# Performance work log

Measured on AMD Instinct MI355X. Metric: run time of the kernel, lower is better.

## Reference

```python
import jax, jax.numpy as jnp
import numpy as np

N_NODES = 200000
N_EDGES = 640000
D_NODE = 128   # NO_NODE_FEATURES_TWO
D_EDGE = 32    # NO_EDGE_FEATURES_TWO
HIDDEN = 128   # HIDDEN_NODE_TWO


def setup_inputs() -> dict:
    key = jax.random.key(0)
    ks = jax.random.split(key, 8)
    x = jax.random.normal(ks[0], (N_NODES, D_NODE), dtype=jnp.float32)
    edge_index = jax.random.randint(ks[1], (2, N_EDGES), 0, N_NODES, dtype=jnp.int64)
    edge_attr = jax.random.normal(ks[2], (N_EDGES, D_EDGE), dtype=jnp.float32)
    u = jax.random.normal(ks[3], (64, D_NODE), dtype=jnp.float32)
    batch = jax.random.randint(ks[4], (N_NODES,), 0, 64, dtype=jnp.int64)
    # Xavier-uniform linear weights (stored as [in, out]); bias filled with 0.01 as in init_weights
    def xavier(k, fan_in, fan_out):
        limit = float(np.sqrt(6.0 / (fan_in + fan_out)))
        return jax.random.uniform(k, (fan_in, fan_out), jnp.float32, -limit, limit)
    W1 = xavier(ks[5], D_EDGE + D_NODE, HIDDEN)          # [160, 128]
    b1 = jnp.full((HIDDEN,), 0.01, dtype=jnp.float32)
    W2 = xavier(ks[6], HIDDEN + D_NODE, D_NODE)          # [256, 128]
    b2 = jnp.full((D_NODE,), 0.01, dtype=jnp.float32)
    return {"x": x, "edge_index": edge_index, "edge_attr": edge_attr,
            "u": u, "batch": batch, "W1": W1, "b1": b1, "W2": W2, "b2": b2}


def reference(x, edge_index, edge_attr, u, batch, W1, b1, W2, b2):
    row, col = edge_index[0], edge_index[1]
    # gather source-node features, concat with edge features: [E, 160]
    msg = jnp.concatenate([x[row], edge_attr], axis=1)
    msg = msg @ W1 + b1                                   # [E, hidden]
    # scatter_add by destination node
    agg = jax.ops.segment_sum(msg, col, num_segments=x.shape[0])  # [N, hidden]
    out = jnp.concatenate([x, agg], axis=1)               # [N, 256]
    return out @ W2 + b2                                  # [N, 128]
```

## Files before the change

kernel.cpp:

```cpp
#include <hip/hip_runtime.h>
#include <hip/hip_bf16.h>

#define N_NODES 200000
#define N_EDGES 640000
#define D_NODE 128
#define D_EDGE 32
#define HIDDEN 128
#define KTOT 288

using bf16x8  = __attribute__((ext_vector_type(8))) short;
using f32x4   = __attribute__((ext_vector_type(4))) float;
using short4v = __attribute__((ext_vector_type(4))) short;

__device__ __forceinline__ short f2b(float f) {
  return __builtin_bit_cast(short, __float2bfloat16(f));
}
__device__ __forceinline__ float b2f(short s) {
  unsigned u = ((unsigned)(unsigned short)s) << 16;
  return __builtin_bit_cast(float, u);
}

__global__ __launch_bounds__(256) void k_prep_x(const float* __restrict__ x,
                                                short* __restrict__ AF) {
  const int i = blockIdx.x * 256 + threadIdx.x;
  const int node = i >> 4;
  const int oct  = (i & 15) << 3;
  const float4 v0 = *(const float4*)&x[(size_t)node * D_NODE + oct];
  const float4 v1 = *(const float4*)&x[(size_t)node * D_NODE + oct + 4];
  bf16x8 o = { f2b(v0.x), f2b(v0.y), f2b(v0.z), f2b(v0.w),
               f2b(v1.x), f2b(v1.y), f2b(v1.z), f2b(v1.w) };
  *(bf16x8*)&AF[(size_t)node * KTOT + oct] = o;
}

__global__ __launch_bounds__(128) void k_prep_wc(const float* __restrict__ W1,
                                                 const float* __restrict__ b1,
                                                 const float* __restrict__ W2,
                                                 short* __restrict__ WcT,
                                                 float* __restrict__ bc) {
  const int b = blockIdx.x;
  const int c = threadIdx.x;
  if (b < 128) {
    WcT[c * KTOT + b] = f2b(W2[b * 128 + c]);
  } else if (b < KTOT) {
    const int i = b - 128;
    float acc = 0.f;
    #pragma unroll 8
    for (int q = 0; q < 128; ++q)
      acc += W1[i * 128 + q] * W2[(128 + q) * 128 + c];
    WcT[c * KTOT + b] = f2b(acc);
  } else {
    float acc = 0.f;
    #pragma unroll 8
    for (int q = 0; q < 128; ++q)
      acc += b1[q] * W2[(128 + q) * 128 + c];
    bc[c] = acc;
  }
}

__global__ __launch_bounds__(256) void k_hist(const int* __restrict__ ei,
                                              int* cnt, int* slot) {
  const int e = blockIdx.x * 256 + threadIdx.x;
  if (e < N_EDGES) slot[e] = atomicAdd(&cnt[ei[N_EDGES + e]], 1);
}

#define SCAN_NB 196

__global__ __launch_bounds__(256) void k_scan_a(const int* __restrict__ cnt,
                                                int* bsum) {
  __shared__ int sh[256];
  const int b = blockIdx.x, t = threadIdx.x;
  const int base = b * 1024 + t * 4;
  int s = 0;
  #pragma unroll
  for (int k = 0; k < 4; ++k) {
    const int idx = base + k;
    s += (idx < N_NODES) ? cnt[idx] : 0;
  }
  sh[t] = s; __syncthreads();
  for (int o = 128; o > 0; o >>= 1) {
    if (t < o) sh[t] += sh[t + o];
    __syncthreads();
  }
  if (t == 0) bsum[b] = sh[0];
}

__global__ __launch_bounds__(256) void k_scan_b(const int* __restrict__ bsum,
                                                int* bpre) {
  __shared__ int sh[256];
  const int t = threadIdx.x;
  const int v0 = (t < SCAN_NB) ? bsum[t] : 0;
  sh[t] = v0; __syncthreads();
  for (int o = 1; o < 256; o <<= 1) {
    const int tv = (t >= o) ? sh[t - o] : 0;
    __syncthreads();
    sh[t] += tv;
    __syncthreads();
  }
  bpre[t] = sh[t] - v0;
}

__global__ __launch_bounds__(256) void k_scan_c(const int* __restrict__ cnt,
                                                const int* __restrict__ bpre,
                                                int* offv) {
  __shared__ int sh[256];
  const int b = blockIdx.x, t = threadIdx.x;
  const int base = b * 1024 + t * 4;
  int v[4], p[4], s = 0;
  #pragma unroll
  for (int k = 0; k < 4; ++k) {
    const int idx = base + k;
    v[k] = (idx < N_NODES) ? cnt[idx] : 0;
    p[k] = s; s += v[k];
  }
  sh[t] = s; __syncthreads();
  const int tot = s;
  for (int o = 1; o < 256; o <<= 1) {
    const int tv = (t >= o) ? sh[t - o] : 0;
    __syncthreads();
    sh[t] += tv;
    __syncthreads();
  }
  const int gb = bpre[b] + (sh[t] - tot);
  #pragma unroll
  for (int k = 0; k < 4; ++k) {
    const int idx = base + k;
    if (idx < N_NODES) offv[idx] = gb + p[k];
  }
}

__global__ __launch_bounds__(256) void k_place2(const int* __restrict__ ei,
                                                const int* __restrict__ offv,
                                                const int* __restrict__ slot,
                                                int* perm, int* rows) {
  const int e = blockIdx.x * 256 + threadIdx.x;
  if (e < N_EDGES) {
    const int j = offv[ei[N_EDGES + e]] + slot[e];
    perm[j] = e;
    rows[j] = ei[e];
  }
}

__global__ __launch_bounds__(256) void k_sagg(
    const float* __restrict__ ea, const int* __restrict__ offv,
    const int* __restrict__ cnt, const int* __restrict__ rows,
    const int* __restrict__ perm, short* __restrict__ AF)
{
  const int gtid = blockIdx.x * 256 + threadIdx.x;
  if (gtid < N_NODES * 16) {
    const int node = gtid >> 4;
    const int oct  = (gtid & 15) << 3;
    const int s0 = offv[node];
    const int s1 = s0 + cnt[node];
    float a[8] = {};
    for (int j = s0; j < s1; ++j) {
      const int row = rows[j];
      const bf16x8 v = *(const bf16x8*)&AF[(size_t)row * KTOT + oct];
      #pragma unroll
      for (int k = 0; k < 8; ++k) a[k] += b2f(v[k]);
    }
    bf16x8 o;
    #pragma unroll
    for (int k = 0; k < 8; ++k) o[k] = f2b(a[k]);
    *(bf16x8*)&AF[(size_t)node * KTOT + 128 + oct] = o;
  } else {
    const int t2 = gtid - N_NODES * 16;
    const int node = t2 >> 3;
    const int q    = (t2 & 7) << 2;
    if (node >= N_NODES) return;
    const int s0 = offv[node];
    const int s1 = s0 + cnt[node];
    float a0 = 0.f, a1 = 0.f, a2 = 0.f, a3 = 0.f;
    for (int j = s0; j < s1; ++j) {
      const int e = perm[j];
      const float4 v = *(const float4*)&ea[(size_t)e * D_EDGE + q];
      a0 += v.x; a1 += v.y; a2 += v.z; a3 += v.w;
    }
    short4v o = { f2b(a0), f2b(a1), f2b(a2), f2b(a3) };
    *(short4v*)&AF[(size_t)node * KTOT + 256 + q] = o;
  }
}

#define LDP 104

__global__ __launch_bounds__(256, 4) void k_out2(
    const short* __restrict__ AF, const short* __restrict__ WcT,
    const float* __restrict__ bc, const float* __restrict__ b2,
    const int* __restrict__ cnt, float* __restrict__ out)
{
  __shared__ short smem[64 * LDP + 128 * LDP];
  short* lA = smem;
  short* lB = smem + 64 * LDP;
  const int tid = threadIdx.x;
  const int n0  = blockIdx.x * 64;

  const int lane = tid & 63;
  const int wid  = tid >> 6;
  const int wm = wid >> 1, wn = wid & 1;
  const int lrow = lane & 15;
  const int lk   = (lane >> 4) << 3;

  f32x4 acc[2][4] = {};

  #pragma unroll
  for (int p = 0; p < 3; ++p) {
    for (int i = tid; i < 1536; i += 256) {
      const int n = i / 12, ck = (i % 12) << 3;
      *(bf16x8*)&lB[n * LDP + ck] = *(const bf16x8*)&WcT[n * KTOT + p * 96 + ck];
    }
    for (int i = tid; i < 768; i += 256) {
      const int m = i / 12, ck = (i % 12) << 3;
      *(bf16x8*)&lA[m * LDP + ck] = *(const bf16x8*)&AF[(size_t)(n0 + m) * KTOT + p * 96 + ck];
    }
    __syncthreads();
    #pragma unroll
    for (int kt = 0; kt < 3; ++kt) {
      const int ks = kt * 32 + lk;
      bf16x8 af[2], bfr[4];
      #pragma unroll
      for (int i = 0; i < 2; ++i)
        af[i]  = *(const bf16x8*)&lA[(wm * 32 + i * 16 + lrow) * LDP + ks];
      #pragma unroll
      for (int j = 0; j < 4; ++j)
        bfr[j] = *(const bf16x8*)&lB[(wn * 64 + j * 16 + lrow) * LDP + ks];
      #pragma unroll
      for (int i = 0; i < 2; ++i)
        #pragma unroll
        for (int j = 0; j < 4; ++j)
          acc[i][j] = __builtin_amdgcn_mfma_f32_16x16x32_bf16(af[i], bfr[j], acc[i][j], 0, 0, 0);
    }
    __syncthreads();
  }

  float* lf = (float*)smem;
  const int rb = wm * 32 + ((lane >> 4) << 2);
  const int cb = wn * 64 + lrow;
  float bcv[4], b2v[4];
  #pragma unroll
  for (int j = 0; j < 4; ++j) {
    bcv[j] = bc[cb + j * 16];
    b2v[j] = b2[cb + j * 16];
  }
  #pragma unroll
  for (int i = 0; i < 2; ++i) {
    #pragma unroll
    for (int r = 0; r < 4; ++r) {
      const int row = rb + i * 16 + r;
      const float cf = (float)cnt[n0 + row];
      #pragma unroll
      for (int j = 0; j < 4; ++j)
        lf[row * 128 + cb + j * 16] = acc[i][j][r] + cf * bcv[j] + b2v[j];
    }
  }
  __syncthreads();
  #pragma unroll
  for (int u = 0; u < 8; ++u) {
    const int idx = tid + u * 256;
    const int row = idx >> 5, f4 = (idx & 31) << 2;
    *(float4*)&out[(size_t)(n0 + row) * HIDDEN + f4] = *(const float4*)&lf[row * 128 + f4];
  }
}

extern "C" void kernel_launch(void* const* d_in, const int* in_sizes, int n_in,
                              void* d_out, int out_size, void* d_ws, size_t ws_size,
                              hipStream_t stream) {
  const float* x  = (const float*)d_in[0];
  const int*   ei = (const int*)d_in[1];
  const float* ea = (const float*)d_in[2];
  const float* W1 = (const float*)d_in[5];
  const float* b1 = (const float*)d_in[6];
  const float* W2 = (const float*)d_in[7];
  const float* b2 = (const float*)d_in[8];
  float* out = (float*)d_out;

  const size_t AF_B   = (size_t)N_NODES * KTOT * 2;
  const size_t WCT_B  = 128 * KTOT * 2;
  const size_t BC_B   = 512;
  const size_t CNT_B  = (size_t)N_NODES * 4;
  const size_t SLOT_B = (size_t)N_EDGES * 4;

  const size_t o_AF   = 0;
  const size_t o_wct  = o_AF + AF_B;
  const size_t o_bc   = o_wct + WCT_B;
  const size_t o_cnt  = o_bc + BC_B;
  const size_t o_off  = o_cnt + CNT_B;
  const size_t o_slot = o_off + CNT_B;
  const size_t o_perm = o_slot + SLOT_B;
  const size_t o_rows = o_perm + SLOT_B;
  const size_t o_bsum = o_rows + SLOT_B;
  const size_t o_bpre = o_bsum + 1024;

  short* AF   = (short*)((char*)d_ws + o_AF);
  short* WcT  = (short*)((char*)d_ws + o_wct);
  float* bc   = (float*)((char*)d_ws + o_bc);
  int*   cnt  = (int*)((char*)d_ws + o_cnt);
  int*   offv = (int*)((char*)d_ws + o_off);
  int*   slot = (int*)((char*)d_ws + o_slot);
  int*   perm = (int*)((char*)d_ws + o_perm);
  int*   rows = (int*)((char*)d_ws + o_rows);
  int*   bsum = (int*)((char*)d_ws + o_bsum);
  int*   bpre = (int*)((char*)d_ws + o_bpre);

  k_prep_x<<<(N_NODES * 16) / 256, 256, 0, stream>>>(x, AF);
  k_prep_wc<<<KTOT + 1, 128, 0, stream>>>(W1, b1, W2, WcT, bc);

  hipMemsetAsync(cnt, 0, CNT_B, stream);
  k_hist <<<(N_EDGES + 255) / 256, 256, 0, stream>>>(ei, cnt, slot);
  k_scan_a<<<SCAN_NB, 256, 0, stream>>>(cnt, bsum);
  k_scan_b<<<1, 256, 0, stream>>>(bsum, bpre);
  k_scan_c<<<SCAN_NB, 256, 0, stream>>>(cnt, bpre, offv);
  k_place2<<<(N_EDGES + 255) / 256, 256, 0, stream>>>(ei, offv, slot, perm, rows);

  k_sagg<<<(N_NODES * 24 + 255) / 256, 256, 0, stream>>>(ea, offv, cnt, rows, perm, AF);
  k_out2<<<N_NODES / 64, 256, 0, stream>>>(AF, WcT, bc, b2, cnt, out);
}
```

Baseline: 233.8 us.

## Fuse neighbor aggregation into output GEMM and merge prep with histogram

The segment-sum gather of neighbor bf16 features and edge attributes now runs inside the output GEMM kernel and writes straight into shared memory. This removes the round-trip through the 288-wide AF staging buffer in global memory and the separate aggregation kernel. The bf16 conversion of x and the destination-count histogram are combined into one launch, and the M-tile shrinks to 32 rows so the larger A tile fits. The cost is that the irregular, degree-dependent gather latency now sits in front of the MFMA work in every block, and occupancy is lower because of more LDS.

```diff
diff --git a/kernel.cpp b/kernel.cpp
--- a/kernel.cpp
+++ b/kernel.cpp
@@ -20,16 +20,27 @@
   return __builtin_bit_cast(float, u);
 }
 
-__global__ __launch_bounds__(256) void k_prep_x(const float* __restrict__ x,
-                                                short* __restrict__ AF) {
-  const int i = blockIdx.x * 256 + threadIdx.x;
-  const int node = i >> 4;
-  const int oct  = (i & 15) << 3;
-  const float4 v0 = *(const float4*)&x[(size_t)node * D_NODE + oct];
-  const float4 v1 = *(const float4*)&x[(size_t)node * D_NODE + oct + 4];
-  bf16x8 o = { f2b(v0.x), f2b(v0.y), f2b(v0.z), f2b(v0.w),
-               f2b(v1.x), f2b(v1.y), f2b(v1.z), f2b(v1.w) };
-  *(bf16x8*)&AF[(size_t)node * KTOT + oct] = o;
+#define PREP_NB 12500
+#define HIST_NB 2500
+
+__global__ __launch_bounds__(256) void k_prep(
+    const float* __restrict__ x, short* __restrict__ xb,
+    const int* __restrict__ ei, int* cnt, int* slot)
+{
+  const int b = blockIdx.x;
+  if (b < PREP_NB) {
+    const int i = b * 256 + threadIdx.x;
+    const int node = i >> 4;
+    const int oct  = (i & 15) << 3;
+    const float4 v0 = *(const float4*)&x[(size_t)node * D_NODE + oct];
+    const float4 v1 = *(const float4*)&x[(size_t)node * D_NODE + oct + 4];
+    bf16x8 o = { f2b(v0.x), f2b(v0.y), f2b(v0.z), f2b(v0.w),
+                 f2b(v1.x), f2b(v1.y), f2b(v1.z), f2b(v1.w) };
+    *(bf16x8*)&xb[(size_t)node * D_NODE + oct] = o;
+  } else {
+    const int e = (b - PREP_NB) * 256 + threadIdx.x;
+    if (e < N_EDGES) slot[e] = atomicAdd(&cnt[ei[N_EDGES + e]], 1);
+  }
 }
 
 __global__ __launch_bounds__(128) void k_prep_wc(const float* __restrict__ W1,
@@ -57,12 +68,6 @@
   }
 }
 
-__global__ __launch_bounds__(256) void k_hist(const int* __restrict__ ei,
-                                              int* cnt, int* slot) {
-  const int e = blockIdx.x * 256 + threadIdx.x;
-  if (e < N_EDGES) slot[e] = atomicAdd(&cnt[ei[N_EDGES + e]], 1);
-}
-
 #define SCAN_NB 196
 
 __global__ __launch_bounds__(256) void k_scan_a(const int* __restrict__ cnt,
@@ -140,58 +145,61 @@
   }
 }
 
-__global__ __launch_bounds__(256) void k_sagg(
-    const float* __restrict__ ea, const int* __restrict__ offv,
-    const int* __restrict__ cnt, const int* __restrict__ rows,
-    const int* __restrict__ perm, short* __restrict__ AF)
+#define BM  32
+#define LDA 296
+#define LDB 104
+
+__global__ __launch_bounds__(256, 3) void k_outF(
+    const short* __restrict__ xb, const float* __restrict__ ea,
+    const int* __restrict__ offv, const int* __restrict__ cnt,
+    const int* __restrict__ rows, const int* __restrict__ perm,
+    const short* __restrict__ WcT, const float* __restrict__ bc,
+    const float* __restrict__ b2, float* __restrict__ out)
 {
-  const int gtid = blockIdx.x * 256 + threadIdx.x;
-  if (gtid < N_NODES * 16) {
-    const int node = gtid >> 4;
-    const int oct  = (gtid & 15) << 3;
-    const int s0 = offv[node];
-    const int s1 = s0 + cnt[node];
-    float a[8] = {};
-    for (int j = s0; j < s1; ++j) {
-      const int row = rows[j];
-      const bf16x8 v = *(const bf16x8*)&AF[(size_t)row * KTOT + oct];
+  __shared__ short sA[BM * LDA];
+  __shared__ short sB[128 * LDB];
+  const int tid = threadIdx.x;
+  const int n0  = blockIdx.x * BM;
+
+  for (int i = tid; i < 1280; i += 256) {
+    if (i < 512) {
+      const int m = i >> 4, oct = (i & 15) << 3;
+      *(bf16x8*)&sA[m * LDA + oct] =
+          *(const bf16x8*)&xb[(size_t)(n0 + m) * D_NODE + oct];
+    } else if (i < 1024) {
+      const int t = i - 512;
+      const int m = t >> 4, oct = (t & 15) << 3;
+      const int s0 = offv[n0 + m];
+      const int s1 = s0 + cnt[n0 + m];
+      float a[8] = {};
+      for (int j = s0; j < s1; ++j) {
+        const bf16x8 v = *(const bf16x8*)&xb[(size_t)rows[j] * D_NODE + oct];
+        #pragma unroll
+        for (int k = 0; k < 8; ++k) a[k] += b2f(v[k]);
+      }
+      bf16x8 o;
       #pragma unroll
-      for (int k = 0; k < 8; ++k) a[k] += b2f(v[k]);
+      for (int k = 0; k < 8; ++k) o[k] = f2b(a[k]);
+      *(bf16x8*)&sA[m * LDA + 128 + oct] = o;
+    } else {
+      const int t = i - 1024;
+      const int m = t >> 3, q = (t & 7) << 2;
+      const int s0 = offv[n0 + m];
+      const int s1 = s0 + cnt[n0 + m];
+      float a0 = 0.f, a1 = 0.f, a2 = 0.f, a3 = 0.f;
+      for (int j = s0; j < s1; ++j) {
+        const float4 v = *(const float4*)&ea[(size_t)perm[j] * D_EDGE + q];
+        a0 += v.x; a1 += v.y; a2 += v.z; a3 += v.w;
+      }
+      short4v o = { f2b(a0), f2b(a1), f2b(a2), f2b(a3) };
+      *(short4v*)&sA[m * LDA + 256 + q] = o;
     }
-    bf16x8 o;
-    #pragma unroll
-    for (int k = 0; k < 8; ++k) o[k] = f2b(a[k]);
-    *(bf16x8*)&AF[(size_t)node * KTOT + 128 + oct] = o;
-  } else {
-    const int t2 = gtid - N_NODES * 16;
-    const int node = t2 >> 3;
-    const int q    = (t2 & 7) << 2;
-    if (node >= N_NODES) return;
-    const int s0 = offv[node];
-    const int s1 = s0 + cnt[node];
-    float a0 = 0.f, a1 = 0.f, a2 = 0.f, a3 = 0.f;
-    for (int j = s0; j < s1; ++j) {
-      const int e = perm[j];
-      const float4 v = *(const float4*)&ea[(size_t)e * D_EDGE + q];
-      a0 += v.x; a1 += v.y; a2 += v.z; a3 += v.w;
-    }
-    short4v o = { f2b(a0), f2b(a1), f2b(a2), f2b(a3) };
-    *(short4v*)&AF[(size_t)node * KTOT + 256 + q] = o;
-  }
-}
-
-#define LDP 104
-
-__global__ __launch_bounds__(256, 4) void k_out2(
-    const short* __restrict__ AF, const short* __restrict__ WcT,
-    const float* __restrict__ bc, const float* __restrict__ b2,
-    const int* __restrict__ cnt, float* __restrict__ out)
-{
-  __shared__ short smem[64 * LDP + 128 * LDP];
-  short* lA = smem;
-  short* lB = smem + 64 * LDP;
-  const int tid = threadIdx.x;
-  const int n0  = blockIdx.x * 64;
+  }
+  for (int i = tid; i < 1536; i += 256) {
+    const int n = i / 12, ck = (i % 12) << 3;
+    *(bf16x8*)&sB[n * LDB + ck] = *(const bf16x8*)&WcT[n * KTOT + ck];
+  }
+  __syncthreads();
 
   const int lane = tid & 63;
   const int wid  = tid >> 6;
@@ -199,40 +207,34 @@
   const int lrow = lane & 15;
   const int lk   = (lane >> 4) << 3;
 
-  f32x4 acc[2][4] = {};
-
+  f32x4 acc[4] = {};
   #pragma unroll
   for (int p = 0; p < 3; ++p) {
-    for (int i = tid; i < 1536; i += 256) {
-      const int n = i / 12, ck = (i % 12) << 3;
-      *(bf16x8*)&lB[n * LDP + ck] = *(const bf16x8*)&WcT[n * KTOT + p * 96 + ck];
-    }
-    for (int i = tid; i < 768; i += 256) {
-      const int m = i / 12, ck = (i % 12) << 3;
-      *(bf16x8*)&lA[m * LDP + ck] = *(const bf16x8*)&AF[(size_t)(n0 + m) * KTOT + p * 96 + ck];
-    }
-    __syncthreads();
     #pragma unroll
     for (int kt = 0; kt < 3; ++kt) {
       const int ks = kt * 32 + lk;
-      bf16x8 af[2], bfr[4];
-      #pragma unroll
-      for (int i = 0; i < 2; ++i)
-        af[i]  = *(const bf16x8*)&lA[(wm * 32 + i * 16 + lrow) * LDP + ks];
+      const bf16x8 af = *(const bf16x8*)&sA[(wm * 16 + lrow) * LDA + p * 96 + ks];
+      bf16x8 bfr[4];
       #pragma unroll
       for (int j = 0; j < 4; ++j)
-        bfr[j] = *(const bf16x8*)&lB[(wn * 64 + j * 16 + lrow) * LDP + ks];
+        bfr[j] = *(const bf16x8*)&sB[(wn * 64 + j * 16 + lrow) * LDB + ks];
       #pragma unroll
-      for (int i = 0; i < 2; ++i)
-        #pragma unroll
-        for (int j = 0; j < 4; ++j)
-          acc[i][j] = __builtin_amdgcn_mfma_f32_16x16x32_bf16(af[i], bfr[j], acc[i][j], 0, 0, 0);
+      for (int j = 0; j < 4; ++j)
+        acc[j] = __builtin_amdgcn_mfma_f32_16x16x32_bf16(af, bfr[j], acc[j], 0, 0, 0);
     }
     __syncthreads();
-  }
-
-  float* lf = (float*)smem;
-  const int rb = wm * 32 + ((lane >> 4) << 2);
+    if (p < 2) {
+      for (int i = tid; i < 1536; i += 256) {
+        const int n = i / 12, ck = (i % 12) << 3;
+        *(bf16x8*)&sB[n * LDB + ck] =
+            *(const bf16x8*)&WcT[n * KTOT + (p + 1) * 96 + ck];
+      }
+      __syncthreads();
+    }
+  }
+
+  float* lf = (float*)sA;
+  const int rb = wm * 16 + ((lane >> 4) << 2);
   const int cb = wn * 64 + lrow;
   float bcv[4], b2v[4];
   #pragma unroll
@@ -241,19 +243,16 @@
     b2v[j] = b2[cb + j * 16];
   }
   #pragma unroll
-  for (int i = 0; i < 2; ++i) {
+  for (int r = 0; r < 4; ++r) {
+    const int row = rb + r;
+    const float cf = (float)cnt[n0 + row];
     #pragma unroll
-    for (int r = 0; r < 4; ++r) {
-      const int row = rb + i * 16 + r;
-      const float cf = (float)cnt[n0 + row];
-      #pragma unroll
-      for (int j = 0; j < 4; ++j)
-        lf[row * 128 + cb + j * 16] = acc[i][j][r] + cf * bcv[j] + b2v[j];
-    }
+    for (int j = 0; j < 4; ++j)
+      lf[row * 128 + cb + j * 16] = acc[j][r] + cf * bcv[j] + b2v[j];
   }
   __syncthreads();
   #pragma unroll
-  for (int u = 0; u < 8; ++u) {
+  for (int u = 0; u < 4; ++u) {
     const int idx = tid + u * 256;
     const int row = idx >> 5, f4 = (idx & 31) << 2;
     *(float4*)&out[(size_t)(n0 + row) * HIDDEN + f4] = *(const float4*)&lf[row * 128 + f4];
@@ -272,14 +271,14 @@
   const float* b2 = (const float*)d_in[8];
   float* out = (float*)d_out;
 
-  const size_t AF_B   = (size_t)N_NODES * KTOT * 2;
+  const size_t XB_B   = (size_t)N_NODES * D_NODE * 2;
   const size_t WCT_B  = 128 * KTOT * 2;
   const size_t BC_B   = 512;
   const size_t CNT_B  = (size_t)N_NODES * 4;
   const size_t SLOT_B = (size_t)N_EDGES * 4;
 
-  const size_t o_AF   = 0;
-  const size_t o_wct  = o_AF + AF_B;
+  const size_t o_xb   = 0;
+  const size_t o_wct  = o_xb + XB_B;
   const size_t o_bc   = o_wct + WCT_B;
   const size_t o_cnt  = o_bc + BC_B;
   const size_t o_off  = o_cnt + CNT_B;
@@ -289,7 +288,7 @@
   const size_t o_bsum = o_rows + SLOT_B;
   const size_t o_bpre = o_bsum + 1024;
 
-  short* AF   = (short*)((char*)d_ws + o_AF);
+  short* xb   = (short*)((char*)d_ws + o_xb);
   short* WcT  = (short*)((char*)d_ws + o_wct);
   float* bc   = (float*)((char*)d_ws + o_bc);
   int*   cnt  = (int*)((char*)d_ws + o_cnt);
@@ -300,16 +299,15 @@
   int*   bsum = (int*)((char*)d_ws + o_bsum);
   int*   bpre = (int*)((char*)d_ws + o_bpre);
 
-  k_prep_x<<<(N_NODES * 16) / 256, 256, 0, stream>>>(x, AF);
+  hipMemsetAsync(cnt, 0, CNT_B, stream);
+  k_prep<<<PREP_NB + HIST_NB, 256, 0, stream>>>(x, xb, ei, cnt, slot);
   k_prep_wc<<<KTOT + 1, 128, 0, stream>>>(W1, b1, W2, WcT, bc);
 
-  hipMemsetAsync(cnt, 0, CNT_B, stream);
-  k_hist <<<(N_EDGES + 255) / 256, 256, 0, stream>>>(ei, cnt, slot);
   k_scan_a<<<SCAN_NB, 256, 0, stream>>>(cnt, bsum);
   k_scan_b<<<1, 256, 0, stream>>>(bsum, bpre);
   k_scan_c<<<SCAN_NB, 256, 0, stream>>>(cnt, bpre, offv);
   k_place2<<<(N_EDGES + 255) / 256, 256, 0, stream>>>(ei, offv, slot, perm, rows);
 
-  k_sagg<<<(N_NODES * 24 + 255) / 256, 256, 0, stream>>>(ea, offv, cnt, rows, perm, AF);
-  k_out2<<<N_NODES / 64, 256, 0, stream>>>(AF, WcT, bc, b2, cnt, out);
-}
+  k_outF<<<N_NODES / BM, 256, 0, stream>>>(xb, ea, offv, cnt, rows, perm,
+                                           WcT, bc, b2, out);
+}
```

New measurement: 307.3 us. 1.31x slower.

## Merge prep kernels, fold scan stage, pack row/perm into int2, unroll gather

Applied to the files above, without the earlier changes.

Fuses the x-to-bf16 conversion, the edge histogram and the weight folding into one launch with block-range dispatch. The single-block scan-b kernel is removed by having each scan-c block reduce its own prefix of block sums. Row and edge indices are packed into one int2 array, and the node gather loop is unrolled by two. Together these aim to cut launch count and serialization and to raise memory-level parallelism in the gather, at the cost of redundant prefix reductions and wider index reads.

```diff
diff --git a/kernel.cpp b/kernel.cpp
--- a/kernel.cpp
+++ b/kernel.cpp
@@ -20,47 +20,53 @@
   return __builtin_bit_cast(float, u);
 }
 
-__global__ __launch_bounds__(256) void k_prep_x(const float* __restrict__ x,
-                                                short* __restrict__ AF) {
-  const int i = blockIdx.x * 256 + threadIdx.x;
-  const int node = i >> 4;
-  const int oct  = (i & 15) << 3;
-  const float4 v0 = *(const float4*)&x[(size_t)node * D_NODE + oct];
-  const float4 v1 = *(const float4*)&x[(size_t)node * D_NODE + oct + 4];
-  bf16x8 o = { f2b(v0.x), f2b(v0.y), f2b(v0.z), f2b(v0.w),
-               f2b(v1.x), f2b(v1.y), f2b(v1.z), f2b(v1.w) };
-  *(bf16x8*)&AF[(size_t)node * KTOT + oct] = o;
-}
-
-__global__ __launch_bounds__(128) void k_prep_wc(const float* __restrict__ W1,
-                                                 const float* __restrict__ b1,
-                                                 const float* __restrict__ W2,
-                                                 short* __restrict__ WcT,
-                                                 float* __restrict__ bc) {
+#define PREP_NB 12500
+#define HIST_NB 2500
+#define WC_NB   145
+
+__global__ __launch_bounds__(256) void k_prep(
+    const float* __restrict__ x, short* __restrict__ AF,
+    const int* __restrict__ ei, int* cnt, int* slot,
+    const float* __restrict__ W1, const float* __restrict__ b1,
+    const float* __restrict__ W2, short* __restrict__ WcT,
+    float* __restrict__ bc)
+{
   const int b = blockIdx.x;
-  const int c = threadIdx.x;
-  if (b < 128) {
-    WcT[c * KTOT + b] = f2b(W2[b * 128 + c]);
-  } else if (b < KTOT) {
-    const int i = b - 128;
-    float acc = 0.f;
-    #pragma unroll 8
-    for (int q = 0; q < 128; ++q)
-      acc += W1[i * 128 + q] * W2[(128 + q) * 128 + c];
-    WcT[c * KTOT + b] = f2b(acc);
+  if (b < PREP_NB) {
+    const int i = b * 256 + threadIdx.x;
+    const int node = i >> 4;
+    const int oct  = (i & 15) << 3;
+    const float4 v0 = *(const float4*)&x[(size_t)node * D_NODE + oct];
+    const float4 v1 = *(const float4*)&x[(size_t)node * D_NODE + oct + 4];
+    bf16x8 o = { f2b(v0.x), f2b(v0.y), f2b(v0.z), f2b(v0.w),
+                 f2b(v1.x), f2b(v1.y), f2b(v1.z), f2b(v1.w) };
+    *(bf16x8*)&AF[(size_t)node * KTOT + oct] = o;
+  } else if (b < PREP_NB + HIST_NB) {
+    const int e = (b - PREP_NB) * 256 + threadIdx.x;
+    slot[e] = atomicAdd(&cnt[ei[N_EDGES + e]], 1);
   } else {
-    float acc = 0.f;
-    #pragma unroll 8
-    for (int q = 0; q < 128; ++q)
-      acc += b1[q] * W2[(128 + q) * 128 + c];
-    bc[c] = acc;
-  }
-}
-
-__global__ __launch_bounds__(256) void k_hist(const int* __restrict__ ei,
-                                              int* cnt, int* slot) {
-  const int e = blockIdx.x * 256 + threadIdx.x;
-  if (e < N_EDGES) slot[e] = atomicAdd(&cnt[ei[N_EDGES + e]], 1);
+    const int t = (b - PREP_NB - HIST_NB) * 256 + threadIdx.x;
+    if (t < 288 * 128) {
+      const int brow = t >> 7, c = t & 127;
+      if (brow < 128) {
+        WcT[c * KTOT + brow] = f2b(W2[brow * 128 + c]);
+      } else {
+        const int i = brow - 128;
+        float acc = 0.f;
+        #pragma unroll 8
+        for (int q = 0; q < 128; ++q)
+          acc += W1[i * 128 + q] * W2[(128 + q) * 128 + c];
+        WcT[c * KTOT + brow] = f2b(acc);
+      }
+    } else if (t < 288 * 128 + 128) {
+      const int c = t - 288 * 128;
+      float acc = 0.f;
+      #pragma unroll 8
+      for (int q = 0; q < 128; ++q)
+        acc += b1[q] * W2[(128 + q) * 128 + c];
+      bc[c] = acc;
+    }
+  }
 }
 
 #define SCAN_NB 196
@@ -84,26 +90,22 @@
   if (t == 0) bsum[b] = sh[0];
 }
 
-__global__ __launch_bounds__(256) void k_scan_b(const int* __restrict__ bsum,
-                                                int* bpre) {
+__global__ __launch_bounds__(256) void k_scan_c2(const int* __restrict__ cnt,
+                                                 const int* __restrict__ bsum,
+                                                 int* offv) {
   __shared__ int sh[256];
-  const int t = threadIdx.x;
-  const int v0 = (t < SCAN_NB) ? bsum[t] : 0;
-  sh[t] = v0; __syncthreads();
-  for (int o = 1; o < 256; o <<= 1) {
-    const int tv = (t >= o) ? sh[t - o] : 0;
-    __syncthreads();
-    sh[t] += tv;
-    __syncthreads();
-  }
-  bpre[t] = sh[t] - v0;
-}
-
-__global__ __launch_bounds__(256) void k_scan_c(const int* __restrict__ cnt,
-                                                const int* __restrict__ bpre,
-                                                int* offv) {
-  __shared__ int sh[256];
+  __shared__ int base_sh;
   const int b = blockIdx.x, t = threadIdx.x;
+
+  sh[t] = (t < SCAN_NB && t < b) ? bsum[t] : 0;
+  __syncthreads();
+  for (int o = 128; o > 0; o >>= 1) {
+    if (t < o) sh[t] += sh[t + o];
+    __syncthreads();
+  }
+  if (t == 0) base_sh = sh[0];
+  __syncthreads();
+
   const int base = b * 1024 + t * 4;
   int v[4], p[4], s = 0;
   #pragma unroll
@@ -120,7 +122,7 @@
     sh[t] += tv;
     __syncthreads();
   }
-  const int gb = bpre[b] + (sh[t] - tot);
+  const int gb = base_sh + (sh[t] - tot);
   #pragma unroll
   for (int k = 0; k < 4; ++k) {
     const int idx = base + k;
@@ -128,22 +130,22 @@
   }
 }
 
-__global__ __launch_bounds__(256) void k_place2(const int* __restrict__ ei,
+__global__ __launch_bounds__(256) void k_place3(const int* __restrict__ ei,
                                                 const int* __restrict__ offv,
                                                 const int* __restrict__ slot,
-                                                int* perm, int* rows) {
+                                                int2* __restrict__ pr) {
   const int e = blockIdx.x * 256 + threadIdx.x;
   if (e < N_EDGES) {
     const int j = offv[ei[N_EDGES + e]] + slot[e];
-    perm[j] = e;
-    rows[j] = ei[e];
+    int2 v; v.x = ei[e]; v.y = e;
+    pr[j] = v;
   }
 }
 
 __global__ __launch_bounds__(256) void k_sagg(
     const float* __restrict__ ea, const int* __restrict__ offv,
-    const int* __restrict__ cnt, const int* __restrict__ rows,
-    const int* __restrict__ perm, short* __restrict__ AF)
+    const int* __restrict__ cnt, const int2* __restrict__ pr,
+    short* __restrict__ AF)
 {
   const int gtid = blockIdx.x * 256 + threadIdx.x;
   if (gtid < N_NODES * 16) {
@@ -152,9 +154,17 @@
     const int s0 = offv[node];
     const int s1 = s0 + cnt[node];
     float a[8] = {};
-    for (int j = s0; j < s1; ++j) {
-      const int row = rows[j];
-      const bf16x8 v = *(const bf16x8*)&AF[(size_t)row * KTOT + oct];
+    int j = s0;
+    for (; j + 1 < s1; j += 2) {
+      const int r0 = pr[j].x;
+      const int r1 = pr[j + 1].x;
+      const bf16x8 v0 = *(const bf16x8*)&AF[(size_t)r0 * KTOT + oct];
+      const bf16x8 v1 = *(const bf16x8*)&AF[(size_t)r1 * KTOT + oct];
+      #pragma unroll
+      for (int k = 0; k < 8; ++k) a[k] += b2f(v0[k]) + b2f(v1[k]);
+    }
+    if (j < s1) {
+      const bf16x8 v = *(const bf16x8*)&AF[(size_t)pr[j].x * KTOT + oct];
       #pragma unroll
       for (int k = 0; k < 8; ++k) a[k] += b2f(v[k]);
     }
@@ -171,8 +181,7 @@
     const int s1 = s0 + cnt[node];
     float a0 = 0.f, a1 = 0.f, a2 = 0.f, a3 = 0.f;
     for (int j = s0; j < s1; ++j) {
-      const int e = perm[j];
-      const float4 v = *(const float4*)&ea[(size_t)e * D_EDGE + q];
+      const float4 v = *(const float4*)&ea[(size_t)pr[j].y * D_EDGE + q];
       a0 += v.x; a1 += v.y; a2 += v.z; a3 += v.w;
     }
     short4v o = { f2b(a0), f2b(a1), f2b(a2), f2b(a3) };
@@ -277,6 +286,7 @@
   const size_t BC_B   = 512;
   const size_t CNT_B  = (size_t)N_NODES * 4;
   const size_t SLOT_B = (size_t)N_EDGES * 4;
+  const size_t PR_B   = (size_t)N_EDGES * 8;
 
   const size_t o_AF   = 0;
   const size_t o_wct  = o_AF + AF_B;
@@ -284,10 +294,8 @@
   const size_t o_cnt  = o_bc + BC_B;
   const size_t o_off  = o_cnt + CNT_B;
   const size_t o_slot = o_off + CNT_B;
-  const size_t o_perm = o_slot + SLOT_B;
-  const size_t o_rows = o_perm + SLOT_B;
-  const size_t o_bsum = o_rows + SLOT_B;
-  const size_t o_bpre = o_bsum + 1024;
+  const size_t o_pr   = o_slot + SLOT_B;
+  const size_t o_bsum = o_pr + PR_B;
 
   short* AF   = (short*)((char*)d_ws + o_AF);
   short* WcT  = (short*)((char*)d_ws + o_wct);
@@ -295,21 +303,17 @@
   int*   cnt  = (int*)((char*)d_ws + o_cnt);
   int*   offv = (int*)((char*)d_ws + o_off);
   int*   slot = (int*)((char*)d_ws + o_slot);
-  int*   perm = (int*)((char*)d_ws + o_perm);
-  int*   rows = (int*)((char*)d_ws + o_rows);
+  int2*  pr   = (int2*)((char*)d_ws + o_pr);
   int*   bsum = (int*)((char*)d_ws + o_bsum);
-  int*   bpre = (int*)((char*)d_ws + o_bpre);
-
-  k_prep_x<<<(N_NODES * 16) / 256, 256, 0, stream>>>(x, AF);
-  k_prep_wc<<<KTOT + 1, 128, 0, stream>>>(W1, b1, W2, WcT, bc);
 
   hipMemsetAsync(cnt, 0, CNT_B, stream);
-  k_hist <<<(N_EDGES + 255) / 256, 256, 0, stream>>>(ei, cnt, slot);
-  k_scan_a<<<SCAN_NB, 256, 0, stream>>>(cnt, bsum);
-  k_scan_b<<<1, 256, 0, stream>>>(bsum, bpre);
-  k_scan_c<<<SCAN_NB, 256, 0, stream>>>(cnt, bpre, offv);
-  k_place2<<<(N_EDGES + 255) / 256, 256, 0, stream>>>(ei, offv, slot, perm, rows);
-
-  k_sagg<<<(N_NODES * 24 + 255) / 256, 256, 0, stream>>>(ea, offv, cnt, rows, perm, AF);
+  k_prep<<<PREP_NB + HIST_NB + WC_NB, 256, 0, stream>>>(
+      x, AF, ei, cnt, slot, W1, b1, W2, WcT, bc);
+
+  k_scan_a <<<SCAN_NB, 256, 0, stream>>>(cnt, bsum);
+  k_scan_c2<<<SCAN_NB, 256, 0, stream>>>(cnt, bsum, offv);
+  k_place3 <<<(N_EDGES + 255) / 256, 256, 0, stream>>>(ei, offv, slot, pr);
+
+  k_sagg<<<(N_NODES * 24 + 255) / 256, 256, 0, stream>>>(ea, offv, cnt, pr, AF);
   k_out2<<<N_NODES / 64, 256, 0, stream>>>(AF, WcT, bc, b2, cnt, out);
 }
```

After: 214.3 us. -8.4%, faster.
